# Performance work log

Measured on AMD Instinct MI355X. Metric: run time of the kernel, lower is better.

Reference implementation:

```python
import jax, jax.numpy as jnp
import numpy as np

M, K, N = 8192, 4096, 4096  # tokens, in_features, out_features


def setup_inputs() -> dict:
    key = jax.random.key(0)
    k1, k2, k3, k4 = jax.random.split(key, 4)
    inp = jax.random.normal(k1, (M, K), dtype=jnp.float32)
    # int8-range weights stored as int32 host-side; [out_features, in_features] like torch Linear
    weight = jax.random.randint(k2, (N, K), -128, 128, dtype=jnp.int32)
    weight_scale = jax.random.uniform(k3, (N,), dtype=jnp.float32, minval=1e-3, maxval=2e-2)
    bias = jax.random.normal(k4, (N,), dtype=jnp.float32)
    return {"input": inp, "weight": weight, "weight_scale": weight_scale, "bias": bias}


def reference(input, weight, weight_scale, bias):
    # --- init-time transforms (W8A8IntLinear.__init__) ---
    wq = weight.T.astype(jnp.int8)                                   # [K, N]
    azp_adj = jnp.sum(wq.astype(jnp.int32), axis=0, keepdims=True)    # [1, N] int32 column sums

    # --- dynamic asymmetric per-token int8 quantization (scaled_int8_quant) ---
    x_max = jnp.max(input, axis=-1, keepdims=True)                    # [M, 1]
    x_min = jnp.min(input, axis=-1, keepdims=True)                    # [M, 1]
    scale = (x_max - x_min) / 255.0                                   # per-token scale
    azp = jnp.round(-128.0 - x_min / scale).astype(jnp.int32)         # per-token zero point
    q = jnp.clip(jnp.round(input / scale).astype(jnp.int32) + azp, -128, 127).astype(jnp.int8)

    # --- int8 GEMM with int32 accumulation (cutlass_scaled_mm_azp) ---
    acc = jnp.matmul(q, wq, preferred_element_type=jnp.int32)         # [M, N] int32
    corrected = (acc - azp * azp_adj).astype(jnp.float32)             # zero-point correction
    return scale * weight_scale[None, :] * corrected + bias[None, :]
```

## Files before the change

### kernel.cpp

```cpp
#include <hip/hip_runtime.h>
#include <cstdint>
#include <cstddef>


#define M_DIM 8192
#define K_DIM 4096
#define N_DIM 4096
#define NT (K_DIM / 64)

typedef int v4i __attribute__((ext_vector_type(4)));

__global__ __launch_bounds__(256) void prep_kernel(
    const float* __restrict__ x, signed char* __restrict__ q,
    float* __restrict__ scale_out, int* __restrict__ azp_out,
    const int* __restrict__ w, signed char* __restrict__ w8,
    int* __restrict__ azp_adj)
{
    const int t = threadIdx.x;
    if (blockIdx.x < M_DIM) {
        const int m = blockIdx.x;
        const float4* row4 = (const float4*)(x + (size_t)m * K_DIM);

        float4 v[4];
        float mx = -3.4e38f, mn = 3.4e38f;
#pragma unroll
        for (int i = 0; i < 4; ++i) {
            v[i] = row4[i * 256 + t];
            mx = fmaxf(mx, fmaxf(fmaxf(v[i].x, v[i].y), fmaxf(v[i].z, v[i].w)));
            mn = fminf(mn, fminf(fminf(v[i].x, v[i].y), fminf(v[i].z, v[i].w)));
        }
#pragma unroll
        for (int off = 32; off; off >>= 1) {
            mx = fmaxf(mx, __shfl_down(mx, off));
            mn = fminf(mn, __shfl_down(mn, off));
        }
        __shared__ float smx[4], smn[4];
        if ((t & 63) == 0) { smx[t >> 6] = mx; smn[t >> 6] = mn; }
        __syncthreads();
        mx = fmaxf(fmaxf(smx[0], smx[1]), fmaxf(smx[2], smx[3]));
        mn = fminf(fminf(smn[0], smn[1]), fminf(smn[2], smn[3]));

        const float scale = (mx - mn) / 255.0f;
        const int azp = (int)rintf(-128.0f - mn / scale);
        if (t == 0) { scale_out[m] = scale; azp_out[m] = azp; }

        int* qrow = (int*)(q + (size_t)m * K_DIM);
        const float* vf = (const float*)v;
#pragma unroll
        for (int i = 0; i < 4; ++i) {
            int b[4];
#pragma unroll
            for (int j = 0; j < 4; ++j) {
                int qv = (int)rintf(vf[4 * i + j] / scale) + azp;
                qv = qv < -128 ? -128 : (qv > 127 ? 127 : qv);
                b[j] = qv;
            }
            qrow[i * 256 + t] =
                (b[0] & 255) | ((b[1] & 255) << 8) | ((b[2] & 255) << 16) | ((b[3] & 255) << 24);
        }
    } else {
        const int n = blockIdx.x - M_DIM;
        const int4* row = (const int4*)(w + (size_t)n * K_DIM);
        int* w8row = (int*)(w8 + (size_t)n * K_DIM);
        int sum = 0;
#pragma unroll
        for (int i = 0; i < 4; ++i) {
            int4 a = row[i * 256 + t];
            sum += a.x + a.y + a.z + a.w;
            w8row[i * 256 + t] =
                (a.x & 255) | ((a.y & 255) << 8) | ((a.z & 255) << 16) | ((a.w & 255) << 24);
        }
#pragma unroll
        for (int off = 32; off; off >>= 1) sum += __shfl_down(sum, off);
        __shared__ int ssum[4];
        if ((t & 63) == 0) ssum[t >> 6] = sum;
        __syncthreads();
        if (t == 0) azp_adj[n] = ssum[0] + ssum[1] + ssum[2] + ssum[3];
    }
}

__device__ __forceinline__ void async_copy16(const signed char* g, signed char* l) {
    __builtin_amdgcn_global_load_lds(
        (const __attribute__((address_space(1))) void*)g,
        (__attribute__((address_space(3))) void*)l, 16, 0, 0);
}

__global__ __launch_bounds__(512, 2) void gemm_kernel(
    const signed char* __restrict__ A,
    const signed char* __restrict__ B,
    const float* __restrict__ scale, const int* __restrict__ azp,
    const int* __restrict__ azp_adj, const float* __restrict__ wscale,
    const float* __restrict__ bias, float* __restrict__ out)
{
    __shared__ signed char sA[4][16384];
    __shared__ signed char sB[4][16384];

    const int t = threadIdx.x;
    const int lane = t & 63;
    const int wave = t >> 6;
    const int quad = lane >> 4;
    const int r16 = lane & 15;

    int bid = blockIdx.y * gridDim.x + blockIdx.x;
    bid = (bid & 7) * 64 + (bid >> 3);
    const int bn = (bid & 15) << 8;
    const int bm = (bid >> 4) << 8;

    const int wm = (wave >> 2) << 7;
    const int wn = (wave & 3) << 6;

    v4i acc[8][4];
#pragma unroll
    for (int i = 0; i < 8; ++i)
#pragma unroll
        for (int j = 0; j < 4; ++j) acc[i][j] = (v4i){0, 0, 0, 0};

    const int srow = t >> 2;
    const int scol = ((t & 3) ^ ((t >> 3) & 3)) << 4;
    const signed char* ag0 = A + (size_t)(bm + srow) * K_DIM + scol;
    const signed char* ag1 = A + (size_t)(bm + 128 + srow) * K_DIM + scol;
    const signed char* bg0 = B + (size_t)(bn + srow) * K_DIM + scol;
    const signed char* bg1 = B + (size_t)(bn + 128 + srow) * K_DIM + scol;

#define STAGE_A(kt) do { const int _b = (kt) & 3; const int _ko = (kt) << 6; \
    async_copy16(ag0 + _ko, &sA[_b][t * 16]); \
    async_copy16(ag1 + _ko, &sA[_b][8192 + t * 16]); } while (0)
#define STAGE_B(kt) do { const int _b = (kt) & 3; const int _ko = (kt) << 6; \
    async_copy16(bg0 + _ko, &sB[_b][t * 16]); \
    async_copy16(bg1 + _ko, &sB[_b][8192 + t * 16]); } while (0)

    STAGE_A(0); STAGE_B(0);
    STAGE_A(1); STAGE_B(1);
    STAGE_A(2); STAGE_B(2);
    asm volatile("s_waitcnt vmcnt(8)" ::: "memory");
    __builtin_amdgcn_s_barrier();

    const int swz = quad ^ ((r16 >> 1) & 3);

    for (int kt = 0; kt < NT; ++kt) {
        const int b = kt & 3;
        const v4i* a4 = (const v4i*)&sA[b][0];
        const v4i* b4 = (const v4i*)&sB[b][0];

        v4i af[4], bf[4];
#pragma unroll
        for (int i = 0; i < 4; ++i) {
            af[i] = a4[(wm + i * 16 + r16) * 4 + swz];
            bf[i] = b4[(wn + i * 16 + r16) * 4 + swz];
        }
        if (kt < NT - 3) STAGE_A(kt + 3);
        asm volatile("" ::: "memory");
        __builtin_amdgcn_s_barrier();
        asm volatile("s_waitcnt lgkmcnt(0)" ::: "memory");
        __builtin_amdgcn_s_setprio(1);
#pragma unroll
        for (int i = 0; i < 4; ++i)
#pragma unroll
            for (int j = 0; j < 4; ++j)
                acc[i][j] = __builtin_amdgcn_mfma_i32_16x16x64_i8(af[i], bf[j], acc[i][j], 0, 0, 0);
        __builtin_amdgcn_s_setprio(0);
        asm volatile("" ::: "memory");
        __builtin_amdgcn_s_barrier();

        v4i ah[4];
#pragma unroll
        for (int i = 0; i < 4; ++i)
            ah[i] = a4[(wm + 64 + i * 16 + r16) * 4 + swz];
        if (kt < NT - 3) STAGE_B(kt + 3);
        asm volatile("" ::: "memory");
        __builtin_amdgcn_s_barrier();
        asm volatile("s_waitcnt lgkmcnt(0)" ::: "memory");
        __builtin_amdgcn_s_setprio(1);
#pragma unroll
        for (int i = 0; i < 4; ++i)
#pragma unroll
            for (int j = 0; j < 4; ++j)
                acc[4 + i][j] = __builtin_amdgcn_mfma_i32_16x16x64_i8(ah[i], bf[j], acc[4 + i][j], 0, 0, 0);
        __builtin_amdgcn_s_setprio(0);

        if (kt < NT - 1) {
            if (kt < NT - 3)        asm volatile("s_waitcnt vmcnt(8)" ::: "memory");
            else if (kt == NT - 3)  asm volatile("s_waitcnt vmcnt(4)" ::: "memory");
            else                    asm volatile("s_waitcnt vmcnt(0)" ::: "memory");
            __builtin_amdgcn_s_barrier();
        }
    }

#undef STAGE_A
#undef STAGE_B

#pragma unroll
    for (int i = 0; i < 8; ++i) {
        const int mbase = bm + wm + i * 16 + quad * 4;
        float sm[4]; int am[4];
#pragma unroll
        for (int r = 0; r < 4; ++r) { sm[r] = scale[mbase + r]; am[r] = azp[mbase + r]; }
#pragma unroll
        for (int j = 0; j < 4; ++j) {
            const int n = bn + wn + j * 16 + r16;
            const float wsn = wscale[n];
            const int adjn = azp_adj[n];
            const float bn_ = bias[n];
#pragma unroll
            for (int r = 0; r < 4; ++r) {
                const int c = acc[i][j][r] - am[r] * adjn;
                out[(size_t)(mbase + r) * N_DIM + n] = sm[r] * wsn * (float)c + bn_;
            }
        }
    }
}

extern "C" void kernel_launch(void* const* d_in, const int* in_sizes, int n_in,
                              void* d_out, int out_size, void* d_ws, size_t ws_size,
                              hipStream_t stream) {
    const float* x      = (const float*)d_in[0];
    const int*   w      = (const int*)d_in[1];
    const float* wscale = (const float*)d_in[2];
    const float* bias   = (const float*)d_in[3];
    float* out = (float*)d_out;

    char* ws = (char*)d_ws;
    signed char* q8  = (signed char*)ws;
    signed char* w8  = (signed char*)(ws + 33554432);
    float* scl       = (float*)(ws + 50331648);
    int*   azp       = (int*)(ws + 50331648 + 32768);
    int*   adj       = (int*)(ws + 50331648 + 65536);

    prep_kernel<<<M_DIM + N_DIM, 256, 0, stream>>>(x, q8, scl, azp, w, w8, adj);
    dim3 grid(N_DIM / 256, M_DIM / 256);
    gemm_kernel<<<grid, 512, 0, stream>>>(q8, w8, scl, azp, adj, wscale, bias, out);
}
```

Before: 410.1 us.

## Restructure GEMM main loop to one barrier per k-tile with peeled tail

Replaces the per-iteration schedule, which used several barriers with interleaved A/B staging between two MFMA halves, with a simpler loop. Each iteration issues both async stage loads up front, runs all 32 MFMAs of the tile, and then waits and synchronises once. The last three tiles are peeled so the loop body has no conditional waits, and LDS addresses are precomputed as base indices. This cuts barrier and wait overhead, but it drops the fine-grained interleaving of LDS reads with MFMAs and raises register pressure because af, bf and ah are all held at once.

```diff
diff --git a/kernel.cpp b/kernel.cpp
--- a/kernel.cpp
+++ b/kernel.cpp
@@ -85,6 +85,30 @@
         (__attribute__((address_space(3))) void*)l, 16, 0, 0);
 }
 
+__device__ __forceinline__ void tile_compute(
+    const v4i* a4, const v4i* b4, int abase, int bbase, v4i (&acc)[8][4])
+{
+    v4i af[4], bf[4], ah[4];
+#pragma unroll
+    for (int i = 0; i < 4; ++i) af[i] = a4[abase + i * 64];
+#pragma unroll
+    for (int i = 0; i < 4; ++i) bf[i] = b4[bbase + i * 64];
+#pragma unroll
+    for (int i = 0; i < 4; ++i) ah[i] = a4[abase + 256 + i * 64];
+    __builtin_amdgcn_s_setprio(1);
+#pragma unroll
+    for (int i = 0; i < 4; ++i)
+#pragma unroll
+        for (int j = 0; j < 4; ++j)
+            acc[i][j] = __builtin_amdgcn_mfma_i32_16x16x64_i8(af[i], bf[j], acc[i][j], 0, 0, 0);
+#pragma unroll
+    for (int i = 0; i < 4; ++i)
+#pragma unroll
+        for (int j = 0; j < 4; ++j)
+            acc[4 + i][j] = __builtin_amdgcn_mfma_i32_16x16x64_i8(ah[i], bf[j], acc[4 + i][j], 0, 0, 0);
+    __builtin_amdgcn_s_setprio(0);
+}
+
 __global__ __launch_bounds__(512, 2) void gemm_kernel(
     const signed char* __restrict__ A,
     const signed char* __restrict__ B,
@@ -129,62 +153,29 @@
     async_copy16(bg0 + _ko, &sB[_b][t * 16]); \
     async_copy16(bg1 + _ko, &sB[_b][8192 + t * 16]); } while (0)
 
+    const int swz = quad ^ ((r16 >> 1) & 3);
+    const v4i* a4 = (const v4i*)&sA[0][0];
+    const v4i* b4 = (const v4i*)&sB[0][0];
+    const int aIdx = (wm + r16) * 4 + swz;
+    const int bIdx = (wn + r16) * 4 + swz;
+
     STAGE_A(0); STAGE_B(0);
     STAGE_A(1); STAGE_B(1);
     STAGE_A(2); STAGE_B(2);
-    asm volatile("s_waitcnt vmcnt(8)" ::: "memory");
-    __builtin_amdgcn_s_barrier();
-
-    const int swz = quad ^ ((r16 >> 1) & 3);
-
-    for (int kt = 0; kt < NT; ++kt) {
-        const int b = kt & 3;
-        const v4i* a4 = (const v4i*)&sA[b][0];
-        const v4i* b4 = (const v4i*)&sB[b][0];
-
-        v4i af[4], bf[4];
-#pragma unroll
-        for (int i = 0; i < 4; ++i) {
-            af[i] = a4[(wm + i * 16 + r16) * 4 + swz];
-            bf[i] = b4[(wn + i * 16 + r16) * 4 + swz];
-        }
-        if (kt < NT - 3) STAGE_A(kt + 3);
-        asm volatile("" ::: "memory");
-        __builtin_amdgcn_s_barrier();
-        asm volatile("s_waitcnt lgkmcnt(0)" ::: "memory");
-        __builtin_amdgcn_s_setprio(1);
-#pragma unroll
-        for (int i = 0; i < 4; ++i)
-#pragma unroll
-            for (int j = 0; j < 4; ++j)
-                acc[i][j] = __builtin_amdgcn_mfma_i32_16x16x64_i8(af[i], bf[j], acc[i][j], 0, 0, 0);
-        __builtin_amdgcn_s_setprio(0);
-        asm volatile("" ::: "memory");
-        __builtin_amdgcn_s_barrier();
-
-        v4i ah[4];
-#pragma unroll
-        for (int i = 0; i < 4; ++i)
-            ah[i] = a4[(wm + 64 + i * 16 + r16) * 4 + swz];
-        if (kt < NT - 3) STAGE_B(kt + 3);
-        asm volatile("" ::: "memory");
-        __builtin_amdgcn_s_barrier();
-        asm volatile("s_waitcnt lgkmcnt(0)" ::: "memory");
-        __builtin_amdgcn_s_setprio(1);
-#pragma unroll
-        for (int i = 0; i < 4; ++i)
-#pragma unroll
-            for (int j = 0; j < 4; ++j)
-                acc[4 + i][j] = __builtin_amdgcn_mfma_i32_16x16x64_i8(ah[i], bf[j], acc[4 + i][j], 0, 0, 0);
-        __builtin_amdgcn_s_setprio(0);
-
-        if (kt < NT - 1) {
-            if (kt < NT - 3)        asm volatile("s_waitcnt vmcnt(8)" ::: "memory");
-            else if (kt == NT - 3)  asm volatile("s_waitcnt vmcnt(4)" ::: "memory");
-            else                    asm volatile("s_waitcnt vmcnt(0)" ::: "memory");
-            __builtin_amdgcn_s_barrier();
-        }
+    asm volatile("s_waitcnt vmcnt(8)\n\ts_barrier" ::: "memory");
+
+    for (int kt = 0; kt < NT - 3; ++kt) {
+        STAGE_A(kt + 3);
+        STAGE_B(kt + 3);
+        const int bb = kt & 3;
+        tile_compute(a4, b4, aIdx + bb * 1024, bIdx + bb * 1024, acc);
+        asm volatile("s_waitcnt vmcnt(8) lgkmcnt(0)\n\ts_barrier" ::: "memory");
     }
+    tile_compute(a4, b4, aIdx + ((NT - 3) & 3) * 1024, bIdx + ((NT - 3) & 3) * 1024, acc);
+    asm volatile("s_waitcnt vmcnt(4) lgkmcnt(0)\n\ts_barrier" ::: "memory");
+    tile_compute(a4, b4, aIdx + ((NT - 2) & 3) * 1024, bIdx + ((NT - 2) & 3) * 1024, acc);
+    asm volatile("s_waitcnt vmcnt(0) lgkmcnt(0)\n\ts_barrier" ::: "memory");
+    tile_compute(a4, b4, aIdx + ((NT - 1) & 3) * 1024, bIdx + ((NT - 1) & 3) * 1024, acc);
 
 #undef STAGE_A
 #undef STAGE_B
```

Measured after the change: 425.3 us. +3.7%, slower.

## Switch GEMM to double-buffered LDS pipeline with higher occupancy bound

Applied to the files above, without the earlier changes.

Replaces the 4-stage LDS ring (prefetch three tiles ahead) with a 2-buffer ping-pong that prefetches the next K tile in each step and waits with vmcnt(0). It also raises launch_bounds min blocks from 2 to 4. Halving LDS per block is meant to let more blocks share a CU and hide latency through occupancy instead of deep prefetch. The tighter register budget implied by the new bound risks spilling the 128-register accumulator array. The shallower prefetch exposes more global-load latency per iteration.

```diff
diff --git a/kernel.cpp b/kernel.cpp
--- a/kernel.cpp
+++ b/kernel.cpp
@@ -85,15 +85,66 @@
         (__attribute__((address_space(3))) void*)l, 16, 0, 0);
 }
 
-__global__ __launch_bounds__(512, 2) void gemm_kernel(
+__device__ __forceinline__ void tile_step(
+    int kt, const v4i* a4, const v4i* b4,
+    signed char* sAd, signed char* sBd,
+    const signed char* ag0, const signed char* ag1,
+    const signed char* bg0, const signed char* bg1,
+    int t, int aIdx, int bIdx, v4i (&acc)[8][4])
+{
+    v4i af[4], bf[4];
+#pragma unroll
+    for (int i = 0; i < 4; ++i) {
+        af[i] = a4[aIdx + i * 64];
+        bf[i] = b4[bIdx + i * 64];
+    }
+    if (kt < NT - 1) {
+        const int ko = (kt + 1) << 6;
+        async_copy16(ag0 + ko, sAd + t * 16);
+        async_copy16(ag1 + ko, sAd + 8192 + t * 16);
+        async_copy16(bg0 + ko, sBd + t * 16);
+        async_copy16(bg1 + ko, sBd + 8192 + t * 16);
+    }
+    __builtin_amdgcn_s_barrier();
+    asm volatile("s_waitcnt lgkmcnt(0)" ::: "memory");
+    __builtin_amdgcn_s_setprio(1);
+#pragma unroll
+    for (int i = 0; i < 4; ++i)
+#pragma unroll
+        for (int j = 0; j < 4; ++j)
+            acc[i][j] = __builtin_amdgcn_mfma_i32_16x16x64_i8(af[i], bf[j], acc[i][j], 0, 0, 0);
+    __builtin_amdgcn_s_setprio(0);
+    __builtin_amdgcn_s_barrier();
+
+    v4i ah[4];
+#pragma unroll
+    for (int i = 0; i < 4; ++i)
+        ah[i] = a4[aIdx + 256 + i * 64];
+    __builtin_amdgcn_s_barrier();
+    asm volatile("s_waitcnt lgkmcnt(0)" ::: "memory");
+    __builtin_amdgcn_s_setprio(1);
+#pragma unroll
+    for (int i = 0; i < 4; ++i)
+#pragma unroll
+        for (int j = 0; j < 4; ++j)
+            acc[4 + i][j] = __builtin_amdgcn_mfma_i32_16x16x64_i8(ah[i], bf[j], acc[4 + i][j], 0, 0, 0);
+    __builtin_amdgcn_s_setprio(0);
+
+    if (kt < NT - 1) {
+        asm volatile("s_waitcnt vmcnt(0)" ::: "memory");
+        __builtin_amdgcn_s_barrier();
+    }
+}
+
+__global__ __launch_bounds__(512, 4) void gemm_kernel(
     const signed char* __restrict__ A,
     const signed char* __restrict__ B,
     const float* __restrict__ scale, const int* __restrict__ azp,
     const int* __restrict__ azp_adj, const float* __restrict__ wscale,
     const float* __restrict__ bias, float* __restrict__ out)
 {
-    __shared__ signed char sA[4][16384];
-    __shared__ signed char sB[4][16384];
+    __shared__ signed char sA[2][16384];
+    __shared__ signed char sB[2][16384];
 
     const int t = threadIdx.x;
     const int lane = t & 63;
@@ -122,72 +173,23 @@
     const signed char* bg0 = B + (size_t)(bn + srow) * K_DIM + scol;
     const signed char* bg1 = B + (size_t)(bn + 128 + srow) * K_DIM + scol;
 
-#define STAGE_A(kt) do { const int _b = (kt) & 3; const int _ko = (kt) << 6; \
-    async_copy16(ag0 + _ko, &sA[_b][t * 16]); \
-    async_copy16(ag1 + _ko, &sA[_b][8192 + t * 16]); } while (0)
-#define STAGE_B(kt) do { const int _b = (kt) & 3; const int _ko = (kt) << 6; \
-    async_copy16(bg0 + _ko, &sB[_b][t * 16]); \
-    async_copy16(bg1 + _ko, &sB[_b][8192 + t * 16]); } while (0)
-
-    STAGE_A(0); STAGE_B(0);
-    STAGE_A(1); STAGE_B(1);
-    STAGE_A(2); STAGE_B(2);
-    asm volatile("s_waitcnt vmcnt(8)" ::: "memory");
-    __builtin_amdgcn_s_barrier();
-
     const int swz = quad ^ ((r16 >> 1) & 3);
-
-    for (int kt = 0; kt < NT; ++kt) {
-        const int b = kt & 3;
-        const v4i* a4 = (const v4i*)&sA[b][0];
-        const v4i* b4 = (const v4i*)&sB[b][0];
-
-        v4i af[4], bf[4];
-#pragma unroll
-        for (int i = 0; i < 4; ++i) {
-            af[i] = a4[(wm + i * 16 + r16) * 4 + swz];
-            bf[i] = b4[(wn + i * 16 + r16) * 4 + swz];
-        }
-        if (kt < NT - 3) STAGE_A(kt + 3);
-        asm volatile("" ::: "memory");
-        __builtin_amdgcn_s_barrier();
-        asm volatile("s_waitcnt lgkmcnt(0)" ::: "memory");
-        __builtin_amdgcn_s_setprio(1);
-#pragma unroll
-        for (int i = 0; i < 4; ++i)
-#pragma unroll
-            for (int j = 0; j < 4; ++j)
-                acc[i][j] = __builtin_amdgcn_mfma_i32_16x16x64_i8(af[i], bf[j], acc[i][j], 0, 0, 0);
-        __builtin_amdgcn_s_setprio(0);
-        asm volatile("" ::: "memory");
-        __builtin_amdgcn_s_barrier();
-
-        v4i ah[4];
-#pragma unroll
-        for (int i = 0; i < 4; ++i)
-            ah[i] = a4[(wm + 64 + i * 16 + r16) * 4 + swz];
-        if (kt < NT - 3) STAGE_B(kt + 3);
-        asm volatile("" ::: "memory");
-        __builtin_amdgcn_s_barrier();
-        asm volatile("s_waitcnt lgkmcnt(0)" ::: "memory");
-        __builtin_amdgcn_s_setprio(1);
-#pragma unroll
-        for (int i = 0; i < 4; ++i)
-#pragma unroll
-            for (int j = 0; j < 4; ++j)
-                acc[4 + i][j] = __builtin_amdgcn_mfma_i32_16x16x64_i8(ah[i], bf[j], acc[4 + i][j], 0, 0, 0);
-        __builtin_amdgcn_s_setprio(0);
-
-        if (kt < NT - 1) {
-            if (kt < NT - 3)        asm volatile("s_waitcnt vmcnt(8)" ::: "memory");
-            else if (kt == NT - 3)  asm volatile("s_waitcnt vmcnt(4)" ::: "memory");
-            else                    asm volatile("s_waitcnt vmcnt(0)" ::: "memory");
-            __builtin_amdgcn_s_barrier();
-        }
-    }
-
-#undef STAGE_A
-#undef STAGE_B
+    const int aIdx = (wm + r16) * 4 + swz;
+    const int bIdx = (wn + r16) * 4 + swz;
+
+    async_copy16(ag0, &sA[0][t * 16]);
+    async_copy16(ag1, &sA[0][8192 + t * 16]);
+    async_copy16(bg0, &sB[0][t * 16]);
+    async_copy16(bg1, &sB[0][8192 + t * 16]);
+    asm volatile("s_waitcnt vmcnt(0)" ::: "memory");
+    __builtin_amdgcn_s_barrier();
+
+    for (int kt = 0; kt < NT; kt += 2) {
+        tile_step(kt,     (const v4i*)&sA[0][0], (const v4i*)&sB[0][0],
+                  &sA[1][0], &sB[1][0], ag0, ag1, bg0, bg1, t, aIdx, bIdx, acc);
+        tile_step(kt + 1, (const v4i*)&sA[1][0], (const v4i*)&sB[1][0],
+                  &sA[0][0], &sB[0][0], ag0, ag1, bg0, bg1, t, aIdx, bIdx, acc);
+    }
 
 #pragma unroll
     for (int i = 0; i < 8; ++i) {
```

New measurement: 1.404 ms. 3.42x slower.
